# Kernel optimization log

Hardware: AMD Instinct MI355X
Metric: run time of the kernel (lower is better)

The kernel has to match this reference:

```python
import jax, jax.numpy as jnp
import numpy as np

N_T, N_S, F_IN, H, N_OUT = 2048, 512, 7, 64, 3


def setup_inputs() -> dict:
    key = jax.random.key(0)
    ks = jax.random.split(key, 12)
    pts = jax.random.normal(ks[0], (N_T, 3), jnp.float32)
    centers = jax.random.normal(ks[1], (N_S, 3), jnp.float32)
    nrm = jax.random.normal(ks[2], (N_S, 3), jnp.float32)
    normals = nrm / jnp.linalg.norm(nrm, axis=-1, keepdims=True)
    areas = jax.random.uniform(ks[3], (N_S,), jnp.float32, 0.1, 1.0)
    ref_lengths = jax.random.uniform(ks[4], (2,), jnp.float32, 0.5, 1.5)

    def lin(k, i, o):
        return jax.random.normal(k, (i, o), jnp.float32) / np.float32(np.sqrt(i))

    return {
        "prediction_points": pts,
        "face_centers": centers,
        "face_normals": normals,
        "face_areas": areas,
        "reference_lengths": ref_lengths,
        "W1": lin(ks[5], F_IN, H), "b1": jnp.zeros((H,), jnp.float32),
        "W2": lin(ks[6], H, H),    "b2": jnp.zeros((H,), jnp.float32),
        "W3": lin(ks[7], H, H),    "b3": jnp.zeros((H,), jnp.float32),
        "Wout": lin(ks[8], H, N_OUT), "bout": jnp.zeros((N_OUT,), jnp.float32),
        "p_scale": jnp.float32(1.0), "p_bias": jnp.float32(0.0),
        "v_scale": jnp.float32(1.0), "v_bias": jnp.float32(0.0),
    }


def reference(prediction_points, face_centers, face_normals, face_areas,
              reference_lengths, W1, b1, W2, b2, W3, b3, Wout, bout,
              p_scale, p_bias, v_scale, v_bias):
    eps = jnp.float32(1e-8)
    # Pairwise relative geometry (translation/rotation-equivariant features).
    rvec = prediction_points[:, None, :] - face_centers[None, :, :]  # [T,S,3]
    r2 = jnp.sum(rvec * rvec, axis=-1)                               # [T,S]
    r = jnp.sqrt(r2 + eps)
    rhat = rvec / r[..., None]
    c = jnp.sum(rhat * face_normals[None, :, :], axis=-1)            # cos(angle)
    # Legendre polynomials P0..P3 (n_spherical_harmonics = 4).
    legendre = jnp.stack(
        [jnp.ones_like(c), c, 0.5 * (3.0 * c * c - 1.0),
         0.5 * (5.0 * c * c * c - 3.0 * c)], axis=-1)                # [T,S,4]
    # Multiscale nondimensional distance features, one per reference length.
    dfeat = 1.0 / (1.0 + r[..., None] / reference_lengths)           # [T,S,2]
    afeat = jnp.broadcast_to(jnp.log(face_areas)[None, :, None],
                             r.shape + (1,))                          # [T,S,1]
    feats = jnp.concatenate([dfeat, legendre, afeat], axis=-1)       # [T,S,7]
    # Kernel MLP evaluated per (target, source) pair.
    h = jnp.tanh(feats @ W1 + b1)
    h = jnp.tanh(h @ W2 + b2)
    h = jnp.tanh(h @ W3 + b3)
    out = h @ Wout + bout                                            # [T,S,3]
    # Green's-function-like decay, area-weighted boundary integral.
    decay = face_areas[None, :] / (r2 + 1.0)                         # [T,S]
    p = jnp.sum(out[..., 0] * decay, axis=1)                         # [T]
    vel = jnp.sum((out[..., 1:2] * rhat
                   + out[..., 2:3] * face_normals[None, :, :])
                  * decay[..., None], axis=1)                        # [T,3]
    pressure = p * p_scale + p_bias
    velocity = vel * v_scale + v_bias
    return jnp.concatenate([pressure[:, None], velocity], axis=-1)   # [T,4]
```

## Files before the change

kernel.cpp:

```cpp
#include <hip/hip_runtime.h>
#include <hip/hip_fp16.h>


#define N_T 2048
#define N_S 512
#define BLK 128
#define SCALE 2.885390081777927f

#define CPY_F 5888
#define CPY_U 1472

typedef _Float16 f16;
typedef _Float16 f16x4 __attribute__((ext_vector_type(4)));
typedef float f32x4 __attribute__((ext_vector_type(4)));
typedef unsigned short u16;
typedef unsigned int u32;

__device__ __forceinline__ float tanh_s(float x) {
    float e = __builtin_amdgcn_exp2f(x);
    return fmaf(-2.0f, __builtin_amdgcn_rcpf(e + 1.0f), 1.0f);
}

__device__ __forceinline__ f32x4 mfma16(f16x4 a, f16x4 b, f32x4 c) {
    return __builtin_amdgcn_mfma_f32_16x16x16f16(a, b, c, 0, 0, 0);
}

__device__ __forceinline__ u32 pkrtz(float a, float b) {
    return __builtin_bit_cast(u32, __builtin_amdgcn_cvt_pkrtz(a, b));
}

__device__ __forceinline__ f16x4 lo4(uint4 g) {
    uint2 p; p.x = g.x; p.y = g.y;
    return __builtin_bit_cast(f16x4, p);
}
__device__ __forceinline__ f16x4 hi4(uint4 g) {
    uint2 p; p.x = g.z; p.y = g.w;
    return __builtin_bit_cast(f16x4, p);
}

__device__ __forceinline__ f16x4 tpack(f32x4 c) {
    uint2 p;
    p.x = pkrtz(tanh_s(c[0]), tanh_s(c[1]));
    p.y = pkrtz(tanh_s(c[2]), tanh_s(c[3]));
    return __builtin_bit_cast(f16x4, p);
}

__global__ __launch_bounds__(256) void prep_kernel(
    const float* __restrict__ W1, const float* __restrict__ b1,
    const float* __restrict__ W2, const float* __restrict__ b2,
    const float* __restrict__ W3, const float* __restrict__ b3,
    const float* __restrict__ Wout, float* __restrict__ ws)
{
    const int tid = blockIdx.x * 256 + threadIdx.x;
    if (tid < 5632) {
        const int cpy = tid / 1408;
        const int r   = tid - cpy * 1408;
        const int u   = r >> 6, lane = r & 63;
        const int q = lane >> 4, l15 = lane & 15;
        float x[8];
        bool lo = false;
        #pragma unroll
        for (int e = 0; e < 8; ++e) {
            const int half = e >> 2, j = e & 3;
            float v;
            if (u < 2) {
                const int mt = u * 2 + half;
                const int k = q * 4 + j;
                v = (k < 7) ? W1[k * 64 + mt * 16 + l15] * SCALE : 0.f;
            } else if (u < 10) {
                const int idx = u - 2, mt = idx >> 1, kp = idx & 1;
                const int k = (kp * 2 + half) * 16 + q * 4 + j;
                v = W2[k * 64 + mt * 16 + l15] * SCALE;
            } else if (u < 18) {
                const int idx = u - 10, mt = idx >> 1, kp = idx & 1;
                const int k = (kp * 2 + half) * 16 + q * 4 + j;
                v = W3[k * 64 + mt * 16 + l15] * SCALE;
            } else {
                const int kp = (u - 18) & 1;
                const int k = (kp * 2 + half) * 16 + q * 4 + j;
                v = (l15 < 3) ? Wout[k * 3 + l15] : 0.f;
                lo = (u >= 20);
            }
            x[e] = v;
        }
        u16 outw[8];
        #pragma unroll
        for (int e = 0; e < 8; ++e) {
            const f16 h = (f16)x[e];
            const f16 val = lo ? (f16)(x[e] - (float)h) : h;
            outw[e] = __builtin_bit_cast(u16, val);
        }
        uint4 g;
        g.x = outw[0] | ((u32)outw[1] << 16);
        g.y = outw[2] | ((u32)outw[3] << 16);
        g.z = outw[4] | ((u32)outw[5] << 16);
        g.w = outw[6] | ((u32)outw[7] << 16);
        *(uint4*)((char*)ws + (size_t)cpy * CPY_F * 4 + (size_t)(u * 64 + lane) * 16) = g;
    } else {
        const int b = tid - 5632;
        const int cpy = b / 192, i = b - cpy * 192;
        const int Lb = i >> 6, j = i & 63;
        float bv;
        if (Lb == 0)      bv = b1[j];
        else if (Lb == 1) bv = b2[j];
        else              bv = b3[j];
        ws[cpy * CPY_F + 5632 + i] = bv * SCALE;
    }
}

__global__ __launch_bounds__(BLK, 2) void globe_mfma(
    const float* __restrict__ pts, const float* __restrict__ ctr,
    const float* __restrict__ nrm, const float* __restrict__ areas,
    const float* __restrict__ rlen, const float* __restrict__ bout,
    const float* __restrict__ p_scale, const float* __restrict__ p_bias,
    const float* __restrict__ v_scale, const float* __restrict__ v_bias,
    const float* __restrict__ ws,
    float* __restrict__ out)
{
    __shared__ __align__(16) u16 featL[2][64][8];
    __shared__ __align__(16) uint4 geomL[2][64];
    __shared__ float xr[4];

    const int tid  = threadIdx.x;
    const int lane = tid & 63;
    const int wv   = tid >> 6;
    const int l15  = lane & 15;
    const int q    = lane >> 4;
    const int qf   = q & 1;
    const int t    = blockIdx.x;

    const float px = pts[3 * t + 0], py = pts[3 * t + 1], pz = pts[3 * t + 2];
    const float invL0 = __builtin_amdgcn_rcpf(rlen[0]);
    const float invL1 = __builtin_amdgcn_rcpf(rlen[1]);
    f32x4 co_init = (f32x4){0.f, 0.f, 0.f, 0.f};
    if (q == 0) { co_init[0] = bout[0]; co_init[1] = bout[1]; co_init[2] = bout[2]; }

    u16 (*ft)[8] = featL[wv];
    uint4* gp = geomL[wv];
    const f16x4 bz = (f16x4){0, 0, 0, 0};
    float accp = 0.f, avx = 0.f, avy = 0.f, avz = 0.f;

    #pragma unroll 1
    for (int ch = 0; ch < 4; ++ch) {
        const uint4* __restrict__ wsU = (const uint4*)ws + ch * CPY_U;
        const float* __restrict__ wsBias = ws + ch * CPY_F + 5632;

        const int s = (wv * 4 + ch) * 64 + lane;
        const float cx = ctr[3 * s + 0], cy = ctr[3 * s + 1], cz = ctr[3 * s + 2];
        const float snx = nrm[3 * s + 0], sny = nrm[3 * s + 1], snz = nrm[3 * s + 2];
        const float ar = areas[s];
        const float rvx = px - cx, rvy = py - cy, rvz = pz - cz;
        const float r2 = rvx * rvx + rvy * rvy + rvz * rvz;
        const float r2e = r2 + 1e-8f;
        const float rinv = __builtin_amdgcn_rsqf(r2e);
        const float r = r2e * rinv;
        const float rhx = rvx * rinv, rhy = rvy * rinv, rhz = rvz * rinv;
        const float cth = rhx * snx + rhy * sny + rhz * snz;
        const float c2 = cth * cth;
        const float decay = ar * __builtin_amdgcn_rcpf(r2 + 1.0f);
        {
            uint4 fw;
            fw.x = pkrtz(__builtin_amdgcn_rcpf(fmaf(r, invL0, 1.0f)),
                         __builtin_amdgcn_rcpf(fmaf(r, invL1, 1.0f)));
            fw.y = pkrtz(1.0f, cth);
            fw.z = pkrtz(fmaf(1.5f, c2, -0.5f), cth * fmaf(2.5f, c2, -1.5f));
            fw.w = pkrtz(__logf(ar), 0.0f);
            *(uint4*)&ft[lane][0] = fw;
        }
        {
            uint4 g;
            g.x = __builtin_bit_cast(u32, decay);
            g.y = pkrtz(rhx, rhy);
            g.z = pkrtz(rhz, snx);
            g.w = pkrtz(sny, snz);
            gp[lane] = g;
        }

        f16x4 B2[4][4];
        {
            const uint4 g0 = wsU[0 * 64 + lane], g1 = wsU[1 * 64 + lane];
            f16x4 a1[4];
            a1[0] = lo4(g0); a1[1] = hi4(g0); a1[2] = lo4(g1); a1[3] = hi4(g1);
            float4 bv[4];
            #pragma unroll
            for (int mt = 0; mt < 4; ++mt)
                bv[mt] = *(const float4*)(wsBias + 0 * 64 + mt * 16 + q * 4);
            #pragma unroll
            for (int n4 = 0; n4 < 4; ++n4) {
                const f16x4 lv = *(const f16x4*)&ft[n4 * 16 + l15][qf * 4];
                const f16x4 bf = (q < 2) ? lv : bz;
                f32x4 c[4];
                #pragma unroll
                for (int mt = 0; mt < 4; ++mt) {
                    c[mt] = (f32x4){bv[mt].x, bv[mt].y, bv[mt].z, bv[mt].w};
                    c[mt] = mfma16(a1[mt], bf, c[mt]);
                }
                #pragma unroll
                for (int mt = 0; mt < 4; ++mt)
                    B2[mt][n4] = tpack(c[mt]);
            }
        }

        f16x4 B3[4][4];
        {
            f16x4 a[4][4];
            #pragma unroll
            for (int mt = 0; mt < 4; ++mt) {
                const uint4 ga = wsU[(2 + 2 * mt) * 64 + lane];
                const uint4 gb = wsU[(3 + 2 * mt) * 64 + lane];
                a[mt][0] = lo4(ga); a[mt][1] = hi4(ga);
                a[mt][2] = lo4(gb); a[mt][3] = hi4(gb);
            }
            float4 bv[4];
            #pragma unroll
            for (int mt = 0; mt < 4; ++mt)
                bv[mt] = *(const float4*)(wsBias + 1 * 64 + mt * 16 + q * 4);
            #pragma unroll
            for (int n4 = 0; n4 < 4; ++n4) {
                f32x4 c[4];
                #pragma unroll
                for (int mt = 0; mt < 4; ++mt)
                    c[mt] = (f32x4){bv[mt].x, bv[mt].y, bv[mt].z, bv[mt].w};
                #pragma unroll
                for (int kt = 0; kt < 4; ++kt)
                    #pragma unroll
                    for (int mt = 0; mt < 4; ++mt)
                        c[mt] = mfma16(a[mt][kt], B2[kt][n4], c[mt]);
                #pragma unroll
                for (int mt = 0; mt < 4; ++mt)
                    B3[mt][n4] = tpack(c[mt]);
            }
        }

        f16x4 BO[4][4];
        {
            f16x4 a[4][4];
            #pragma unroll
            for (int mt = 0; mt < 4; ++mt) {
                const uint4 ga = wsU[(10 + 2 * mt) * 64 + lane];
                const uint4 gb = wsU[(11 + 2 * mt) * 64 + lane];
                a[mt][0] = lo4(ga); a[mt][1] = hi4(ga);
                a[mt][2] = lo4(gb); a[mt][3] = hi4(gb);
            }
            float4 bv[4];
            #pragma unroll
            for (int mt = 0; mt < 4; ++mt)
                bv[mt] = *(const float4*)(wsBias + 2 * 64 + mt * 16 + q * 4);
            #pragma unroll
            for (int n4 = 0; n4 < 4; ++n4) {
                f32x4 c[4];
                #pragma unroll
                for (int mt = 0; mt < 4; ++mt)
                    c[mt] = (f32x4){bv[mt].x, bv[mt].y, bv[mt].z, bv[mt].w};
                #pragma unroll
                for (int kt = 0; kt < 4; ++kt)
                    #pragma unroll
                    for (int mt = 0; mt < 4; ++mt)
                        c[mt] = mfma16(a[mt][kt], B3[kt][n4], c[mt]);
                #pragma unroll
                for (int mt = 0; mt < 4; ++mt)
                    BO[mt][n4] = tpack(c[mt]);
            }
        }

        {
            const uint4 gh0 = wsU[18 * 64 + lane], gh1 = wsU[19 * 64 + lane];
            const uint4 gl0 = wsU[20 * 64 + lane], gl1 = wsU[21 * 64 + lane];
            f16x4 aoh[4], aol[4];
            aoh[0] = lo4(gh0); aoh[1] = hi4(gh0); aoh[2] = lo4(gh1); aoh[3] = hi4(gh1);
            aol[0] = lo4(gl0); aol[1] = hi4(gl0); aol[2] = lo4(gl1); aol[3] = hi4(gl1);
            #pragma unroll
            for (int n4 = 0; n4 < 4; ++n4) {
                f32x4 co = co_init;
                #pragma unroll
                for (int kt = 0; kt < 4; ++kt) {
                    co = mfma16(aoh[kt], BO[kt][n4], co);
                    co = mfma16(aol[kt], BO[kt][n4], co);
                }
                if (q == 0) {
                    const uint4 g = gp[n4 * 16 + l15];
                    const float d = __builtin_bit_cast(float, g.x);
                    const float2 rxy = __half22float2(__builtin_bit_cast(__half2, g.y));
                    const float2 rzx = __half22float2(__builtin_bit_cast(__half2, g.z));
                    const float2 nyz = __half22float2(__builtin_bit_cast(__half2, g.w));
                    const float o0 = co[0], o1 = co[1], o2 = co[2];
                    accp = fmaf(o0, d, accp);
                    avx  = fmaf(fmaf(o1, rxy.x, o2 * rzx.y), d, avx);
                    avy  = fmaf(fmaf(o1, rxy.y, o2 * nyz.x), d, avy);
                    avz  = fmaf(fmaf(o1, rzx.x, o2 * nyz.y), d, avz);
                }
            }
        }
    }

    #pragma unroll
    for (int off = 8; off > 0; off >>= 1) {
        accp += __shfl_down(accp, off);
        avx  += __shfl_down(avx,  off);
        avy  += __shfl_down(avy,  off);
        avz  += __shfl_down(avz,  off);
    }

    if (wv == 1 && lane == 0) {
        xr[0] = accp; xr[1] = avx; xr[2] = avy; xr[3] = avz;
    }
    __syncthreads();
    if (wv == 0 && lane == 0) {
        accp += xr[0]; avx += xr[1]; avy += xr[2]; avz += xr[3];
        const float ps = p_scale[0], pb = p_bias[0];
        const float vs = v_scale[0], vb = v_bias[0];
        out[4 * t + 0] = fmaf(accp, ps, pb);
        out[4 * t + 1] = fmaf(avx, vs, vb);
        out[4 * t + 2] = fmaf(avy, vs, vb);
        out[4 * t + 3] = fmaf(avz, vs, vb);
    }
}

extern "C" void kernel_launch(void* const* d_in, const int* in_sizes, int n_in,
                              void* d_out, int out_size, void* d_ws, size_t ws_size,
                              hipStream_t stream) {
    (void)in_sizes; (void)n_in; (void)ws_size; (void)out_size;
    const float* pts   = (const float*)d_in[0];
    const float* ctr   = (const float*)d_in[1];
    const float* nrm   = (const float*)d_in[2];
    const float* areas = (const float*)d_in[3];
    const float* rlen  = (const float*)d_in[4];
    const float* W1    = (const float*)d_in[5];
    const float* b1    = (const float*)d_in[6];
    const float* W2    = (const float*)d_in[7];
    const float* b2    = (const float*)d_in[8];
    const float* W3    = (const float*)d_in[9];
    const float* b3    = (const float*)d_in[10];
    const float* Wout  = (const float*)d_in[11];
    const float* bout  = (const float*)d_in[12];
    const float* ps    = (const float*)d_in[13];
    const float* pb    = (const float*)d_in[14];
    const float* vs    = (const float*)d_in[15];
    const float* vb    = (const float*)d_in[16];
    float* ws = (float*)d_ws;

    prep_kernel<<<25, 256, 0, stream>>>(W1, b1, W2, b2, W3, b3, Wout, ws);
    globe_mfma<<<N_T, BLK, 0, stream>>>(
        pts, ctr, nrm, areas, rlen, bout, ps, pb, vs, vb, ws, (float*)d_out);
}
```

Baseline: 154.6 us.

## Process two source chunks per iteration to reuse MLP weight fragments

Each wave now handles two 64-source sub-tiles per loop iteration, halving the outer trip count. The weight A-fragments loaded from the workspace are reused across both sub-tiles, and MFMAs for the two sub-tiles are interleaved so independent chains hide MFMA latency. It doubles the register footprint of the activation fragments (B2/B3/BO) and LDS staging, which risks spills or lower occupancy under launch_bounds(128,2). Only the weight copies for chunks 0 and 2 are now read.

```diff
diff --git a/kernel.cpp b/kernel.cpp
--- a/kernel.cpp
+++ b/kernel.cpp
@@ -117,8 +117,8 @@
     const float* __restrict__ ws,
     float* __restrict__ out)
 {
-    __shared__ __align__(16) u16 featL[2][64][8];
-    __shared__ __align__(16) uint4 geomL[2][64];
+    __shared__ __align__(16) u16 featL[2][2][64][8];
+    __shared__ __align__(16) uint4 geomL[2][2][64];
     __shared__ float xr[4];
 
     const int tid  = threadIdx.x;
@@ -135,48 +135,45 @@
     f32x4 co_init = (f32x4){0.f, 0.f, 0.f, 0.f};
     if (q == 0) { co_init[0] = bout[0]; co_init[1] = bout[1]; co_init[2] = bout[2]; }
 
-    u16 (*ft)[8] = featL[wv];
-    uint4* gp = geomL[wv];
     const f16x4 bz = (f16x4){0, 0, 0, 0};
     float accp = 0.f, avx = 0.f, avy = 0.f, avz = 0.f;
 
     #pragma unroll 1
-    for (int ch = 0; ch < 4; ++ch) {
-        const uint4* __restrict__ wsU = (const uint4*)ws + ch * CPY_U;
-        const float* __restrict__ wsBias = ws + ch * CPY_F + 5632;
-
-        const int s = (wv * 4 + ch) * 64 + lane;
-        const float cx = ctr[3 * s + 0], cy = ctr[3 * s + 1], cz = ctr[3 * s + 2];
-        const float snx = nrm[3 * s + 0], sny = nrm[3 * s + 1], snz = nrm[3 * s + 2];
-        const float ar = areas[s];
-        const float rvx = px - cx, rvy = py - cy, rvz = pz - cz;
-        const float r2 = rvx * rvx + rvy * rvy + rvz * rvz;
-        const float r2e = r2 + 1e-8f;
-        const float rinv = __builtin_amdgcn_rsqf(r2e);
-        const float r = r2e * rinv;
-        const float rhx = rvx * rinv, rhy = rvy * rinv, rhz = rvz * rinv;
-        const float cth = rhx * snx + rhy * sny + rhz * snz;
-        const float c2 = cth * cth;
-        const float decay = ar * __builtin_amdgcn_rcpf(r2 + 1.0f);
-        {
+    for (int ch = 0; ch < 2; ++ch) {
+        const uint4* __restrict__ wsU = (const uint4*)ws + (ch * 2) * CPY_U;
+        const float* __restrict__ wsBias = ws + (ch * 2) * CPY_F + 5632;
+
+        #pragma unroll
+        for (int st = 0; st < 2; ++st) {
+            const int s = (wv * 4 + ch * 2 + st) * 64 + lane;
+            const float cx = ctr[3 * s + 0], cy = ctr[3 * s + 1], cz = ctr[3 * s + 2];
+            const float snx = nrm[3 * s + 0], sny = nrm[3 * s + 1], snz = nrm[3 * s + 2];
+            const float ar = areas[s];
+            const float rvx = px - cx, rvy = py - cy, rvz = pz - cz;
+            const float r2 = rvx * rvx + rvy * rvy + rvz * rvz;
+            const float r2e = r2 + 1e-8f;
+            const float rinv = __builtin_amdgcn_rsqf(r2e);
+            const float r = r2e * rinv;
+            const float rhx = rvx * rinv, rhy = rvy * rinv, rhz = rvz * rinv;
+            const float cth = rhx * snx + rhy * sny + rhz * snz;
+            const float c2 = cth * cth;
+            const float decay = ar * __builtin_amdgcn_rcpf(r2 + 1.0f);
             uint4 fw;
             fw.x = pkrtz(__builtin_amdgcn_rcpf(fmaf(r, invL0, 1.0f)),
                          __builtin_amdgcn_rcpf(fmaf(r, invL1, 1.0f)));
             fw.y = pkrtz(1.0f, cth);
             fw.z = pkrtz(fmaf(1.5f, c2, -0.5f), cth * fmaf(2.5f, c2, -1.5f));
             fw.w = pkrtz(__logf(ar), 0.0f);
-            *(uint4*)&ft[lane][0] = fw;
-        }
-        {
+            *(uint4*)&featL[wv][st][lane][0] = fw;
             uint4 g;
             g.x = __builtin_bit_cast(u32, decay);
             g.y = pkrtz(rhx, rhy);
             g.z = pkrtz(rhz, snx);
             g.w = pkrtz(sny, snz);
-            gp[lane] = g;
-        }
-
-        f16x4 B2[4][4];
+            geomL[wv][st][lane] = g;
+        }
+
+        f16x4 B2[2][4][4];
         {
             const uint4 g0 = wsU[0 * 64 + lane], g1 = wsU[1 * 64 + lane];
             f16x4 a1[4];
@@ -187,21 +184,29 @@
                 bv[mt] = *(const float4*)(wsBias + 0 * 64 + mt * 16 + q * 4);
             #pragma unroll
             for (int n4 = 0; n4 < 4; ++n4) {
-                const f16x4 lv = *(const f16x4*)&ft[n4 * 16 + l15][qf * 4];
-                const f16x4 bf = (q < 2) ? lv : bz;
-                f32x4 c[4];
-                #pragma unroll
-                for (int mt = 0; mt < 4; ++mt) {
-                    c[mt] = (f32x4){bv[mt].x, bv[mt].y, bv[mt].z, bv[mt].w};
-                    c[mt] = mfma16(a1[mt], bf, c[mt]);
-                }
-                #pragma unroll
-                for (int mt = 0; mt < 4; ++mt)
-                    B2[mt][n4] = tpack(c[mt]);
-            }
-        }
-
-        f16x4 B3[4][4];
+                f16x4 bf[2];
+                #pragma unroll
+                for (int st = 0; st < 2; ++st) {
+                    const f16x4 lv = *(const f16x4*)&featL[wv][st][n4 * 16 + l15][qf * 4];
+                    bf[st] = (q < 2) ? lv : bz;
+                }
+                f32x4 c[2][4];
+                #pragma unroll
+                for (int mt = 0; mt < 4; ++mt) {
+                    c[0][mt] = (f32x4){bv[mt].x, bv[mt].y, bv[mt].z, bv[mt].w};
+                    c[1][mt] = c[0][mt];
+                    c[0][mt] = mfma16(a1[mt], bf[0], c[0][mt]);
+                    c[1][mt] = mfma16(a1[mt], bf[1], c[1][mt]);
+                }
+                #pragma unroll
+                for (int mt = 0; mt < 4; ++mt) {
+                    B2[0][mt][n4] = tpack(c[0][mt]);
+                    B2[1][mt][n4] = tpack(c[1][mt]);
+                }
+            }
+        }
+
+        f16x4 B3[2][4][4];
         {
             f16x4 a[4][4];
             #pragma unroll
@@ -217,22 +222,28 @@
                 bv[mt] = *(const float4*)(wsBias + 1 * 64 + mt * 16 + q * 4);
             #pragma unroll
             for (int n4 = 0; n4 < 4; ++n4) {
-                f32x4 c[4];
-                #pragma unroll
-                for (int mt = 0; mt < 4; ++mt)
-                    c[mt] = (f32x4){bv[mt].x, bv[mt].y, bv[mt].z, bv[mt].w};
+                f32x4 c[2][4];
+                #pragma unroll
+                for (int mt = 0; mt < 4; ++mt) {
+                    c[0][mt] = (f32x4){bv[mt].x, bv[mt].y, bv[mt].z, bv[mt].w};
+                    c[1][mt] = c[0][mt];
+                }
                 #pragma unroll
                 for (int kt = 0; kt < 4; ++kt)
                     #pragma unroll
-                    for (int mt = 0; mt < 4; ++mt)
-                        c[mt] = mfma16(a[mt][kt], B2[kt][n4], c[mt]);
-                #pragma unroll
-                for (int mt = 0; mt < 4; ++mt)
-                    B3[mt][n4] = tpack(c[mt]);
-            }
-        }
-
-        f16x4 BO[4][4];
+                    for (int mt = 0; mt < 4; ++mt) {
+                        c[0][mt] = mfma16(a[mt][kt], B2[0][kt][n4], c[0][mt]);
+                        c[1][mt] = mfma16(a[mt][kt], B2[1][kt][n4], c[1][mt]);
+                    }
+                #pragma unroll
+                for (int mt = 0; mt < 4; ++mt) {
+                    B3[0][mt][n4] = tpack(c[0][mt]);
+                    B3[1][mt][n4] = tpack(c[1][mt]);
+                }
+            }
+        }
+
+        f16x4 BO[2][4][4];
         {
             f16x4 a[4][4];
             #pragma unroll
@@ -248,18 +259,24 @@
                 bv[mt] = *(const float4*)(wsBias + 2 * 64 + mt * 16 + q * 4);
             #pragma unroll
             for (int n4 = 0; n4 < 4; ++n4) {
-                f32x4 c[4];
-                #pragma unroll
-                for (int mt = 0; mt < 4; ++mt)
-                    c[mt] = (f32x4){bv[mt].x, bv[mt].y, bv[mt].z, bv[mt].w};
+                f32x4 c[2][4];
+                #pragma unroll
+                for (int mt = 0; mt < 4; ++mt) {
+                    c[0][mt] = (f32x4){bv[mt].x, bv[mt].y, bv[mt].z, bv[mt].w};
+                    c[1][mt] = c[0][mt];
+                }
                 #pragma unroll
                 for (int kt = 0; kt < 4; ++kt)
                     #pragma unroll
-                    for (int mt = 0; mt < 4; ++mt)
-                        c[mt] = mfma16(a[mt][kt], B3[kt][n4], c[mt]);
-                #pragma unroll
-                for (int mt = 0; mt < 4; ++mt)
-                    BO[mt][n4] = tpack(c[mt]);
+                    for (int mt = 0; mt < 4; ++mt) {
+                        c[0][mt] = mfma16(a[mt][kt], B3[0][kt][n4], c[0][mt]);
+                        c[1][mt] = mfma16(a[mt][kt], B3[1][kt][n4], c[1][mt]);
+                    }
+                #pragma unroll
+                for (int mt = 0; mt < 4; ++mt) {
+                    BO[0][mt][n4] = tpack(c[0][mt]);
+                    BO[1][mt][n4] = tpack(c[1][mt]);
+                }
             }
         }
 
@@ -271,23 +288,29 @@
             aol[0] = lo4(gl0); aol[1] = hi4(gl0); aol[2] = lo4(gl1); aol[3] = hi4(gl1);
             #pragma unroll
             for (int n4 = 0; n4 < 4; ++n4) {
-                f32x4 co = co_init;
+                f32x4 co[2];
+                co[0] = co_init; co[1] = co_init;
                 #pragma unroll
                 for (int kt = 0; kt < 4; ++kt) {
-                    co = mfma16(aoh[kt], BO[kt][n4], co);
-                    co = mfma16(aol[kt], BO[kt][n4], co);
+                    co[0] = mfma16(aoh[kt], BO[0][kt][n4], co[0]);
+                    co[1] = mfma16(aoh[kt], BO[1][kt][n4], co[1]);
+                    co[0] = mfma16(aol[kt], BO[0][kt][n4], co[0]);
+                    co[1] = mfma16(aol[kt], BO[1][kt][n4], co[1]);
                 }
                 if (q == 0) {
-                    const uint4 g = gp[n4 * 16 + l15];
-                    const float d = __builtin_bit_cast(float, g.x);
-                    const float2 rxy = __half22float2(__builtin_bit_cast(__half2, g.y));
-                    const float2 rzx = __half22float2(__builtin_bit_cast(__half2, g.z));
-                    const float2 nyz = __half22float2(__builtin_bit_cast(__half2, g.w));
-                    const float o0 = co[0], o1 = co[1], o2 = co[2];
-                    accp = fmaf(o0, d, accp);
-                    avx  = fmaf(fmaf(o1, rxy.x, o2 * rzx.y), d, avx);
-                    avy  = fmaf(fmaf(o1, rxy.y, o2 * nyz.x), d, avy);
-                    avz  = fmaf(fmaf(o1, rzx.x, o2 * nyz.y), d, avz);
+                    #pragma unroll
+                    for (int st = 0; st < 2; ++st) {
+                        const uint4 g = geomL[wv][st][n4 * 16 + l15];
+                        const float d = __builtin_bit_cast(float, g.x);
+                        const float2 rxy = __half22float2(__builtin_bit_cast(__half2, g.y));
+                        const float2 rzx = __half22float2(__builtin_bit_cast(__half2, g.z));
+                        const float2 nyz = __half22float2(__builtin_bit_cast(__half2, g.w));
+                        const float o0 = co[st][0], o1 = co[st][1], o2 = co[st][2];
+                        accp = fmaf(o0, d, accp);
+                        avx  = fmaf(fmaf(o1, rxy.x, o2 * rzx.y), d, avx);
+                        avy  = fmaf(fmaf(o1, rxy.y, o2 * nyz.x), d, avy);
+                        avz  = fmaf(fmaf(o1, rzx.x, o2 * nyz.y), d, avz);
+                    }
                 }
             }
         }
```

After: 143.5 us. 1.08x faster.
